# Optimization experiments

Measured on AMD Instinct MI355X. Metric: run time of the kernel, lower is better.

Reference implementation:

```python
import jax, jax.numpy as jnp
import numpy as np

INPUT, OUTPUT, HIDDEN, EMBED = 20000, 2048, 1024, 512
BATCH, NUM_GENES = 512, 20000

def _linear_init(key, fan_in, fan_out):
    kw, kb = jax.random.split(key)
    bound = 1.0 / np.sqrt(fan_in)
    W = jax.random.uniform(kw, (fan_out, fan_in), minval=-bound, maxval=bound, dtype=jnp.float32)
    b = jax.random.uniform(kb, (fan_out,), minval=-bound, maxval=bound, dtype=jnp.float32)
    return W, b

def setup_inputs() -> dict:
    key = jax.random.key(0)
    kx, ke, k1, k2, k3 = jax.random.split(key, 5)
    x = jax.random.normal(kx, (BATCH, INPUT), dtype=jnp.float32)
    embedding_x = jax.random.normal(ke, (NUM_GENES, EMBED), dtype=jnp.float32)
    W_ge, b_ge = _linear_init(k1, INPUT, HIDDEN)   # gene_expander Linear
    W_em, b_em = _linear_init(k2, EMBED, HIDDEN)   # embed_mlp Linear
    W_c, b_c = _linear_init(k3, 2 * HIDDEN, OUTPUT)  # combiner Linear
    return {"x": x, "embedding_x": embedding_x, "W_ge": W_ge, "b_ge": b_ge,
            "W_em": W_em, "b_em": b_em, "W_c": W_c, "b_c": b_c}

def reference(x, embedding_x, W_ge, b_ge, W_em, b_em, W_c, b_c):
    lrelu = lambda v: jax.nn.leaky_relu(v, negative_slope=0.01)
    # gene_expander: [B, input] -> [B, hidden]
    x_expanded = lrelu(x @ W_ge.T + b_ge)
    # embed_mlp (dropout = identity at eval): [G, embed] -> [G, hidden]
    gene_embeddings = lrelu(embedding_x @ W_em.T + b_em)
    # softmax over features, then batched GEMM replaces the per-sample loop
    num_genes = min(x.shape[1], gene_embeddings.shape[0])
    weights = jax.nn.softmax(x, axis=1)
    weighted_embeddings = weights[:, :num_genes] @ gene_embeddings[:num_genes]  # [B, hidden]
    combined = jnp.concatenate([x_expanded, weighted_embeddings], axis=1)  # [B, 2*hidden]
    return lrelu(combined @ W_c.T + b_c)  # [B, output]
```

## Files before the change

### kernel.cpp

```cpp
#include <hip/hip_runtime.h>
#include <hip/hip_bf16.h>
#include <stdint.h>

#define BATCH  512
#define INPUT  20000
#define KPAD   20032
#define NPADE  20224
#define HIDDEN 1024
#define EMBED  512
#define NOUT   2048

typedef __attribute__((ext_vector_type(8))) __bf16 bf16x8;
typedef __attribute__((ext_vector_type(8))) unsigned short u16x8;
typedef __attribute__((ext_vector_type(4))) unsigned short u16x4;
typedef __attribute__((ext_vector_type(4))) float f32x4;

static __device__ __forceinline__ unsigned short f2bf(float f) {
  uint32_t u = __builtin_bit_cast(uint32_t, f);
  u += 0x7fffu + ((u >> 16) & 1u);
  return (unsigned short)(u >> 16);
}

static __device__ __forceinline__ void g2l16(const unsigned short* g, unsigned short* l) {
  __builtin_amdgcn_global_load_lds(
      (const __attribute__((address_space(1))) void*)g,
      (__attribute__((address_space(3))) void*)l, 16, 0, 0);
}

#define MFMA(a, b, c) __builtin_amdgcn_mfma_f32_16x16x32_bf16((a), (b), (c), 0, 0, 0)

template<int EPI>
__global__ __launch_bounds__(512, 2) void gemm8r(
    const unsigned short* __restrict__ A0p, const unsigned short* __restrict__ B0p,
    const unsigned short* __restrict__ A1p, const unsigned short* __restrict__ B1p,
    int lda, int ldb,
    const float* __restrict__ bias,
    void* __restrict__ Cp, int ldc,
    int Nv, int Nw, int K, int kChunk)
{
  __shared__ __align__(16) unsigned short As[2][2][128 * 64];
  __shared__ __align__(16) unsigned short Bs[2][2][128 * 64];
  unsigned short* AsW = &As[0][0][0];
  unsigned short* BsW = &Bs[0][0][0];

  const int zall  = blockIdx.z;
  const int which = (EPI == 1) ? (zall >> 4) : 0;
  const int z     = (EPI == 1) ? (zall & 15) : 0;
  const unsigned short* Ap = which ? A1p : A0p;
  const unsigned short* Bp = which ? B1p : B0p;

  const int m0 = blockIdx.y * 256, n0 = blockIdx.x * 256;
  const int k0   = z * kChunk;
  const int kend = min(K, k0 + kChunk);
  const int nt   = (kend - k0) >> 6;

  const int tid = threadIdx.x;
  const int l = tid & 63, w = tid >> 6;
  const int srow = tid >> 3;
  const int sc8  = tid & 7;
  const unsigned short* agl = Ap + (size_t)(m0 + srow) * lda + k0 + sc8 * 8;
  const unsigned short* bgl = Bp + (size_t)(n0 + srow) * ldb + k0 + sc8 * 8;
  const int swc = ((sc8 ^ (srow & 7)) << 3);

  const int wr = w >> 2, wc = w & 3;
  const int lr = l & 15, lk = (l >> 4) * 8;
  const int xorv = (lr & 7) * 8;
  const int c0 = lk ^ xorv;
  const int c1 = (32 + lk) ^ xorv;

  auto ldsA = [&](int buf, int r) -> unsigned short* {
    return AsW + (buf * 2 + (r >> 7)) * 8192 + (r & 127) * 64 + swc;
  };
  auto ldsB = [&](int buf, int r) -> unsigned short* {
    return BsW + (buf * 2 + (r >> 7)) * 8192 + (r & 127) * 64 + swc;
  };
  auto rdA = [&](int buf, int mi, int ks) -> bf16x8 {
    return *reinterpret_cast<const bf16x8*>(
        AsW + (buf * 2 + wr) * 8192 + (mi * 16 + lr) * 64 + (ks ? c1 : c0));
  };
  auto rdB = [&](int buf, int ni, int ks) -> bf16x8 {
    return *reinterpret_cast<const bf16x8*>(
        BsW + (buf * 2 + (wc >> 1)) * 8192 + ((wc & 1) * 64 + ni * 16 + lr) * 64 + (ks ? c1 : c0));
  };

  f32x4 acc[8][4] = {};

  u16x8 ra0, ra1, ra2, ra3, rb0, rb1, rb2, rb3;

#define LOADT(dk)                                                            \
  do {                                                                       \
    ra0 = *reinterpret_cast<const u16x8*>(agl + (size_t)0   * lda + (dk));   \
    ra1 = *reinterpret_cast<const u16x8*>(agl + (size_t)64  * lda + (dk));   \
    ra2 = *reinterpret_cast<const u16x8*>(agl + (size_t)128 * lda + (dk));   \
    ra3 = *reinterpret_cast<const u16x8*>(agl + (size_t)192 * lda + (dk));   \
    rb0 = *reinterpret_cast<const u16x8*>(bgl + (size_t)0   * ldb + (dk));   \
    rb1 = *reinterpret_cast<const u16x8*>(bgl + (size_t)64  * ldb + (dk));   \
    rb2 = *reinterpret_cast<const u16x8*>(bgl + (size_t)128 * ldb + (dk));   \
    rb3 = *reinterpret_cast<const u16x8*>(bgl + (size_t)192 * ldb + (dk));   \
  } while (0)

#define WRITET(buf)                                                          \
  do {                                                                       \
    *reinterpret_cast<u16x8*>(ldsA(buf, srow))       = ra0;                  \
    *reinterpret_cast<u16x8*>(ldsA(buf, srow + 64))  = ra1;                  \
    *reinterpret_cast<u16x8*>(ldsA(buf, srow + 128)) = ra2;                  \
    *reinterpret_cast<u16x8*>(ldsA(buf, srow + 192)) = ra3;                  \
    *reinterpret_cast<u16x8*>(ldsB(buf, srow))       = rb0;                  \
    *reinterpret_cast<u16x8*>(ldsB(buf, srow + 64))  = rb1;                  \
    *reinterpret_cast<u16x8*>(ldsB(buf, srow + 128)) = rb2;                  \
    *reinterpret_cast<u16x8*>(ldsB(buf, srow + 192)) = rb3;                  \
  } while (0)

  LOADT(0);
  WRITET(0);
  __syncthreads();

  for (int t = 0; t < nt; ++t) {
    const int buf = t & 1, nb = buf ^ 1;
    if (t + 1 < nt) LOADT((t + 1) << 6);
    __builtin_amdgcn_sched_barrier(0);

    bf16x8 a[8][2], b[4][2];
#pragma unroll
    for (int mi = 0; mi < 8; ++mi) { a[mi][0] = rdA(buf, mi, 0); a[mi][1] = rdA(buf, mi, 1); }
#pragma unroll
    for (int ni = 0; ni < 4; ++ni) { b[ni][0] = rdB(buf, ni, 0); b[ni][1] = rdB(buf, ni, 1); }
#pragma unroll
    for (int mi = 0; mi < 8; ++mi)
#pragma unroll
      for (int ni = 0; ni < 4; ++ni) {
        acc[mi][ni] = MFMA(a[mi][0], b[ni][0], acc[mi][ni]);
        acc[mi][ni] = MFMA(a[mi][1], b[ni][1], acc[mi][ni]);
      }

    if (t + 1 < nt) WRITET(nb);
    __syncthreads();
  }
#undef LOADT
#undef WRITET

  const int rb_ = (l >> 4) * 4;
#pragma unroll
  for (int mi = 0; mi < 8; ++mi)
#pragma unroll
    for (int ni = 0; ni < 4; ++ni)
#pragma unroll
      for (int j = 0; j < 4; ++j) {
        int m = m0 + wr * 128 + mi * 16 + rb_ + j;
        int n = n0 + wc * 64 + ni * 16 + lr;
        float v = acc[mi][ni][j];
        if (EPI == 0) {
          if (n < Nw) {
            float t2 = v + bias[m];
            t2 = t2 > 0.f ? t2 : 0.01f * t2;
            reinterpret_cast<unsigned short*>(Cp)[(size_t)m * ldc + n] =
                (n < Nv) ? f2bf(t2) : (unsigned short)0;
          }
        } else {
          reinterpret_cast<float*>(Cp)[(size_t)z * (BATCH * NOUT) + (size_t)m * ldc +
                                       which * 1024 + n] = v;
        }
      }
}

template<int EPI>
__global__ __launch_bounds__(256) void gemm97(
    const unsigned short* __restrict__ A, const unsigned short* __restrict__ B,
    int lda, int ldb,
    const float* __restrict__ bias,
    void* __restrict__ Cp, int ldc, int pstride,
    int M, int N, int Nw, int K, int kChunk)
{
  __shared__ __align__(16) unsigned short As[128 * 64];
  __shared__ __align__(16) unsigned short Bs[128 * 64];

  const int z = blockIdx.z;
  const int m0 = blockIdx.y * 128, n0 = blockIdx.x * 128;
  const int k0   = z * kChunk;
  const int kend = min(K, k0 + kChunk);
  const int tid = threadIdx.x;
  const int l = tid & 63, w = tid >> 6;

  const int srow = w * 32 + (l >> 3);
  const int scol = (l & 7) * 8;
  const unsigned short* ag = A + (size_t)(m0 + srow) * lda + scol;
  const unsigned short* bg = B + (size_t)(n0 + srow) * ldb + scol;

  const int wm = (w >> 1) * 64, wn = (w & 1) * 64;
  const int lr = l & 15, lk = (l >> 4) * 8;

  f32x4 acc[4][4] = {};

  for (int kb = k0; kb < kend; kb += 64) {
#pragma unroll
    for (int j = 0; j < 4; ++j)
      g2l16(ag + (size_t)j * 8 * lda + kb, As + (w * 32 + j * 8) * 64);
#pragma unroll
    for (int j = 0; j < 4; ++j)
      g2l16(bg + (size_t)j * 8 * ldb + kb, Bs + (w * 32 + j * 8) * 64);
    __syncthreads();
#pragma unroll
    for (int ks = 0; ks < 2; ++ks) {
      bf16x8 a[4], b[4];
#pragma unroll
      for (int i = 0; i < 4; ++i)
        a[i] = *reinterpret_cast<const bf16x8*>(&As[(wm + i * 16 + lr) * 64 + ks * 32 + lk]);
#pragma unroll
      for (int i = 0; i < 4; ++i)
        b[i] = *reinterpret_cast<const bf16x8*>(&Bs[(wn + i * 16 + lr) * 64 + ks * 32 + lk]);
#pragma unroll
      for (int mi = 0; mi < 4; ++mi)
#pragma unroll
        for (int ni = 0; ni < 4; ++ni)
          acc[mi][ni] = MFMA(a[mi], b[ni], acc[mi][ni]);
    }
    __syncthreads();
  }

  const int rb = (l >> 4) * 4;
#pragma unroll
  for (int mi = 0; mi < 4; ++mi) {
#pragma unroll
    for (int ni = 0; ni < 4; ++ni) {
#pragma unroll
      for (int j = 0; j < 4; ++j) {
        int m = m0 + wm + mi * 16 + rb + j;
        int n = n0 + wn + ni * 16 + lr;
        float v = acc[mi][ni][j];
        if (EPI == 0) {
          if (n < Nw) {
            float t = v + bias[m];
            t = t > 0.f ? t : 0.01f * t;
            reinterpret_cast<unsigned short*>(Cp)[(size_t)m * ldc + n] =
                (n < N) ? f2bf(t) : (unsigned short)0;
          }
        } else {
          reinterpret_cast<float*>(Cp)[(size_t)z * pstride + (size_t)m * ldc + n] = v;
        }
      }
    }
  }
}

__global__ __launch_bounds__(256) void convert_kernel(
    const float* __restrict__ src, unsigned short* __restrict__ dst,
    int rows, int cols, int rowsPad, int colsPad)
{
  const int cpc = colsPad >> 3;
  const int nchunks = rowsPad * cpc;
  for (int idx = blockIdx.x * 256 + threadIdx.x; idx < nchunks; idx += gridDim.x * 256) {
    int row = idx / cpc;
    int c0  = (idx - row * cpc) << 3;
    u16x8 v = {};
    if (row < rows && c0 < cols) {
      const float* p = src + (size_t)row * cols + c0;
      f32x4 f0 = *reinterpret_cast<const f32x4*>(p);
      f32x4 f1 = *reinterpret_cast<const f32x4*>(p + 4);
      v[0] = f2bf(f0[0]); v[1] = f2bf(f0[1]); v[2] = f2bf(f0[2]); v[3] = f2bf(f0[3]);
      v[4] = f2bf(f1[0]); v[5] = f2bf(f1[1]); v[6] = f2bf(f1[2]); v[7] = f2bf(f1[3]);
    }
    *reinterpret_cast<u16x8*>(dst + (size_t)row * colsPad + c0) = v;
  }
}

__global__ __launch_bounds__(256) void prep_x_kernel(
    const float* __restrict__ x,
    unsigned short* __restrict__ xb,
    unsigned short* __restrict__ wb)
{
  const int r = blockIdx.x;
  const int t = threadIdx.x;
  const float* xr = x + (size_t)r * INPUT;

  float m = -3.4e38f, s = 0.f;
  for (int c = t; c < INPUT / 4; c += 256) {
    float4 v = reinterpret_cast<const float4*>(xr)[c];
    float cm = fmaxf(fmaxf(v.x, v.y), fmaxf(v.z, v.w));
    if (cm > m) { s *= __expf(m - cm); m = cm; }
    s += __expf(v.x - m) + __expf(v.y - m) + __expf(v.z - m) + __expf(v.w - m);
  }
#pragma unroll
  for (int off = 32; off > 0; off >>= 1) {
    float om = __shfl_xor(m, off);
    float os = __shfl_xor(s, off);
    float nm = fmaxf(m, om);
    s = s * __expf(m - nm) + os * __expf(om - nm);
    m = nm;
  }
  __shared__ float sm[4], ss[4];
  if ((t & 63) == 0) { sm[t >> 6] = m; ss[t >> 6] = s; }
  __syncthreads();
  float M4 = fmaxf(fmaxf(sm[0], sm[1]), fmaxf(sm[2], sm[3]));
  float S4 = ss[0] * __expf(sm[0] - M4) + ss[1] * __expf(sm[1] - M4)
           + ss[2] * __expf(sm[2] - M4) + ss[3] * __expf(sm[3] - M4);
  float inv = 1.f / S4;

  unsigned short* xbr = xb + (size_t)r * KPAD;
  unsigned short* wbr = wb + (size_t)r * KPAD;
  for (int c = t; c < KPAD / 4; c += 256) {
    u16x4 xo = {}, wo = {};
    if (c < INPUT / 4) {
      float4 v = reinterpret_cast<const float4*>(xr)[c];
      xo[0] = f2bf(v.x); xo[1] = f2bf(v.y); xo[2] = f2bf(v.z); xo[3] = f2bf(v.w);
      wo[0] = f2bf(__expf(v.x - M4) * inv);
      wo[1] = f2bf(__expf(v.y - M4) * inv);
      wo[2] = f2bf(__expf(v.z - M4) * inv);
      wo[3] = f2bf(__expf(v.w - M4) * inv);
    }
    reinterpret_cast<u16x4*>(xbr)[c] = xo;
    reinterpret_cast<u16x4*>(wbr)[c] = wo;
  }
}

template<int S, int MODE>
__global__ __launch_bounds__(256) void reduce_kernel(
    const float* __restrict__ P, const float* __restrict__ bias, void* __restrict__ outp)
{
  size_t base = ((size_t)blockIdx.x * 256 + threadIdx.x) * 4;
  f32x4 s = {};
#pragma unroll
  for (int zz = 0; zz < S; ++zz)
    s += *reinterpret_cast<const f32x4*>(P + (size_t)zz * BATCH * NOUT + base);
  int n = (int)(base & (NOUT - 1));
  if (MODE == 0) {
    u16x4 o;
    if (n < 1024) {
#pragma unroll
      for (int j = 0; j < 4; ++j) {
        float v = s[j] + bias[n + j];
        v = v > 0.f ? v : 0.01f * v;
        o[j] = f2bf(v);
      }
    } else {
#pragma unroll
      for (int j = 0; j < 4; ++j) o[j] = f2bf(s[j]);
    }
    *reinterpret_cast<u16x4*>(reinterpret_cast<unsigned short*>(outp) + base) = o;
  } else {
    f32x4 o;
#pragma unroll
    for (int j = 0; j < 4; ++j) {
      float v = s[j] + bias[n + j];
      o[j] = v > 0.f ? v : 0.01f * v;
    }
    *reinterpret_cast<f32x4*>(reinterpret_cast<float*>(outp) + base) = o;
  }
}

extern "C" void kernel_launch(void* const* d_in, const int* in_sizes, int n_in,
                              void* d_out, int out_size, void* d_ws, size_t ws_size,
                              hipStream_t stream)
{
  const float* x    = (const float*)d_in[0];
  const float* emb  = (const float*)d_in[1];
  const float* W_ge = (const float*)d_in[2];
  const float* b_ge = (const float*)d_in[3];
  const float* W_em = (const float*)d_in[4];
  const float* b_em = (const float*)d_in[5];
  const float* W_c  = (const float*)d_in[6];
  const float* b_c  = (const float*)d_in[7];
  float* out = (float*)d_out;

  char* ws = (char*)d_ws;
  unsigned short* xb   = (unsigned short*)(ws);
  unsigned short* wb   = (unsigned short*)(ws + 20512768);
  unsigned short* Wgeb = (unsigned short*)(ws + 41025536);
  unsigned short* Et   = (unsigned short*)(ws + 82051072);
  unsigned short* Wcb  = (unsigned short*)(ws + 123076608);
  unsigned short* comb = (unsigned short*)(ws + 131465216);
  float*          P    = (float*)(ws + 133562368);
  unsigned short* embb = (unsigned short*)(ws + 133562368);
  unsigned short* Wemb = (unsigned short*)(ws + 133562368 + 20709376);

  convert_kernel<<<1024, 256, 0, stream>>>(emb,  embb, INPUT, EMBED, NPADE, EMBED);
  convert_kernel<<<256,  256, 0, stream>>>(W_em, Wemb, HIDDEN, EMBED, HIDDEN, EMBED);
  convert_kernel<<<1024, 256, 0, stream>>>(W_ge, Wgeb, HIDDEN, INPUT, HIDDEN, KPAD);
  convert_kernel<<<512,  256, 0, stream>>>(W_c,  Wcb,  NOUT, NOUT, NOUT, NOUT);

  prep_x_kernel<<<BATCH, 256, 0, stream>>>(x, xb, wb);

  gemm8r<0><<<dim3(79, 4, 1), 512, 0, stream>>>(
      Wemb, embb, nullptr, nullptr, EMBED, EMBED, b_em,
      Et, KPAD, INPUT, KPAD, EMBED, EMBED);

  gemm8r<1><<<dim3(4, 2, 32), 512, 0, stream>>>(
      xb, Wgeb, wb, Et, KPAD, KPAD, nullptr,
      P, NOUT, 0, 0, KPAD, 1280);

  reduce_kernel<16, 0><<<(BATCH * NOUT / 4) / 256, 256, 0, stream>>>(P, b_ge, comb);

  gemm97<1><<<dim3(16, 4, 4), 256, 0, stream>>>(
      comb, Wcb, NOUT, NOUT, nullptr,
      P, NOUT, BATCH * NOUT, BATCH, NOUT, NOUT, NOUT, 512);

  reduce_kernel<4, 1><<<(BATCH * NOUT / 4) / 256, 256, 0, stream>>>(P, b_c, out);
}
```

Before: 241.7 us.

## Template GEMM on BK, remap blocks per XCD, and double-buffer register prefetch

Replaces the fixed 256x256x64 GEMM kernel with a template over K-tile depth and occupancy. It uses a 1D grid whose block index is remapped so tiles that share operands land on the same XCD. The main loop is unrolled by two with two register staging sets, so the global loads for tile t+2 are issued while tile t computes, and MFMA sections are wrapped in s_setprio. The embedding GEMM now uses BK=32 with 4 waves per SIMD. This adds register pressure and more complex code, and the XCD remap assumes round-robin dispatch of blocks across the 8 XCDs.

```diff
diff --git a/kernel.cpp b/kernel.cpp
--- a/kernel.cpp
+++ b/kernel.cpp
@@ -29,8 +29,8 @@
 
 #define MFMA(a, b, c) __builtin_amdgcn_mfma_f32_16x16x32_bf16((a), (b), (c), 0, 0, 0)
 
-template<int EPI>
-__global__ __launch_bounds__(512, 2) void gemm8r(
+template<int EPI, int BK, int MW>
+__global__ __launch_bounds__(512, MW) void gemmT(
     const unsigned short* __restrict__ A0p, const unsigned short* __restrict__ B0p,
     const unsigned short* __restrict__ A1p, const unsigned short* __restrict__ B1p,
     int lda, int ldb,
@@ -38,106 +38,118 @@
     void* __restrict__ Cp, int ldc,
     int Nv, int Nw, int K, int kChunk)
 {
-  __shared__ __align__(16) unsigned short As[2][2][128 * 64];
-  __shared__ __align__(16) unsigned short Bs[2][2][128 * 64];
-  unsigned short* AsW = &As[0][0][0];
-  unsigned short* BsW = &Bs[0][0][0];
-
-  const int zall  = blockIdx.z;
-  const int which = (EPI == 1) ? (zall >> 4) : 0;
-  const int z     = (EPI == 1) ? (zall & 15) : 0;
+  constexpr int CPR = BK / 8;
+  constexpr int RPP = 512 / CPR;
+  constexpr int NP  = 256 / RPP;
+  constexpr int KS  = BK / 32;
+  constexpr int XM  = CPR - 1;
+
+  __shared__ __align__(16) unsigned short AsW[2 * 256 * BK];
+  __shared__ __align__(16) unsigned short BsW[2 * 256 * BK];
+
+  const int b = blockIdx.x;
+  const int xcd = b & 7, rank = b >> 3;
+  int m0, n0, z = 0, which = 0;
+  if (EPI == 1) {
+    int g  = xcd + 8 * (rank >> 3);
+    int mm = rank & 7;
+    which = g >> 4; z = g & 15;
+    n0 = (mm >> 1) * 256; m0 = (mm & 1) * 256;
+  } else {
+    int x  = xcd + 8 * (rank >> 2);
+    int mm = rank & 3;
+    int nx = (Nw + 255) >> 8;
+    if (x >= nx) return;
+    n0 = x * 256; m0 = mm * 256;
+  }
   const unsigned short* Ap = which ? A1p : A0p;
   const unsigned short* Bp = which ? B1p : B0p;
 
-  const int m0 = blockIdx.y * 256, n0 = blockIdx.x * 256;
   const int k0   = z * kChunk;
   const int kend = min(K, k0 + kChunk);
-  const int nt   = (kend - k0) >> 6;
+  const int nt   = (kend - k0) / BK;
 
   const int tid = threadIdx.x;
   const int l = tid & 63, w = tid >> 6;
-  const int srow = tid >> 3;
-  const int sc8  = tid & 7;
+  const int srow = tid / CPR;
+  const int sc8  = tid % CPR;
   const unsigned short* agl = Ap + (size_t)(m0 + srow) * lda + k0 + sc8 * 8;
   const unsigned short* bgl = Bp + (size_t)(n0 + srow) * ldb + k0 + sc8 * 8;
-  const int swc = ((sc8 ^ (srow & 7)) << 3);
+  const int swc = ((sc8 ^ (srow & XM)) << 3);
 
   const int wr = w >> 2, wc = w & 3;
-  const int lr = l & 15, lk = (l >> 4) * 8;
-  const int xorv = (lr & 7) * 8;
-  const int c0 = lk ^ xorv;
-  const int c1 = (32 + lk) ^ xorv;
-
-  auto ldsA = [&](int buf, int r) -> unsigned short* {
-    return AsW + (buf * 2 + (r >> 7)) * 8192 + (r & 127) * 64 + swc;
-  };
-  auto ldsB = [&](int buf, int r) -> unsigned short* {
-    return BsW + (buf * 2 + (r >> 7)) * 8192 + (r & 127) * 64 + swc;
-  };
-  auto rdA = [&](int buf, int mi, int ks) -> bf16x8 {
-    return *reinterpret_cast<const bf16x8*>(
-        AsW + (buf * 2 + wr) * 8192 + (mi * 16 + lr) * 64 + (ks ? c1 : c0));
-  };
-  auto rdB = [&](int buf, int ni, int ks) -> bf16x8 {
-    return *reinterpret_cast<const bf16x8*>(
-        BsW + (buf * 2 + (wc >> 1)) * 8192 + ((wc & 1) * 64 + ni * 16 + lr) * 64 + (ks ? c1 : c0));
-  };
+  const int lr = l & 15, lkc = l >> 4;
 
   f32x4 acc[8][4] = {};
-
-  u16x8 ra0, ra1, ra2, ra3, rb0, rb1, rb2, rb3;
-
-#define LOADT(dk)                                                            \
-  do {                                                                       \
-    ra0 = *reinterpret_cast<const u16x8*>(agl + (size_t)0   * lda + (dk));   \
-    ra1 = *reinterpret_cast<const u16x8*>(agl + (size_t)64  * lda + (dk));   \
-    ra2 = *reinterpret_cast<const u16x8*>(agl + (size_t)128 * lda + (dk));   \
-    ra3 = *reinterpret_cast<const u16x8*>(agl + (size_t)192 * lda + (dk));   \
-    rb0 = *reinterpret_cast<const u16x8*>(bgl + (size_t)0   * ldb + (dk));   \
-    rb1 = *reinterpret_cast<const u16x8*>(bgl + (size_t)64  * ldb + (dk));   \
-    rb2 = *reinterpret_cast<const u16x8*>(bgl + (size_t)128 * ldb + (dk));   \
-    rb3 = *reinterpret_cast<const u16x8*>(bgl + (size_t)192 * ldb + (dk));   \
+  u16x8 rA[2][NP], rB[2][NP];
+
+#define LOADS(S, dk)                                                           \
+  do {                                                                         \
+    _Pragma("unroll")                                                          \
+    for (int p = 0; p < NP; ++p) {                                             \
+      rA[S][p] = *reinterpret_cast<const u16x8*>(agl + (size_t)(p * RPP) * lda + (dk)); \
+      rB[S][p] = *reinterpret_cast<const u16x8*>(bgl + (size_t)(p * RPP) * ldb + (dk)); \
+    }                                                                          \
   } while (0)
 
-#define WRITET(buf)                                                          \
-  do {                                                                       \
-    *reinterpret_cast<u16x8*>(ldsA(buf, srow))       = ra0;                  \
-    *reinterpret_cast<u16x8*>(ldsA(buf, srow + 64))  = ra1;                  \
-    *reinterpret_cast<u16x8*>(ldsA(buf, srow + 128)) = ra2;                  \
-    *reinterpret_cast<u16x8*>(ldsA(buf, srow + 192)) = ra3;                  \
-    *reinterpret_cast<u16x8*>(ldsB(buf, srow))       = rb0;                  \
-    *reinterpret_cast<u16x8*>(ldsB(buf, srow + 64))  = rb1;                  \
-    *reinterpret_cast<u16x8*>(ldsB(buf, srow + 128)) = rb2;                  \
-    *reinterpret_cast<u16x8*>(ldsB(buf, srow + 192)) = rb3;                  \
+#define WRITES(S, BUF)                                                         \
+  do {                                                                         \
+    _Pragma("unroll")                                                          \
+    for (int p = 0; p < NP; ++p) {                                             \
+      *reinterpret_cast<u16x8*>(AsW + (BUF) * (256 * BK) + (srow + p * RPP) * BK + swc) = rA[S][p]; \
+      *reinterpret_cast<u16x8*>(BsW + (BUF) * (256 * BK) + (srow + p * RPP) * BK + swc) = rB[S][p]; \
+    }                                                                          \
   } while (0)
 
-  LOADT(0);
-  WRITET(0);
+#define COMPUTE(BUF)                                                           \
+  do {                                                                         \
+    _Pragma("unroll")                                                          \
+    for (int ks = 0; ks < KS; ++ks) {                                          \
+      bf16x8 af[8], bg_[4];                                                    \
+      _Pragma("unroll")                                                        \
+      for (int mi = 0; mi < 8; ++mi) {                                         \
+        int ck = (ks * 4 + lkc) ^ (lr & XM);                                   \
+        af[mi] = *reinterpret_cast<const bf16x8*>(                             \
+            AsW + (BUF) * (256 * BK) + (wr * 128 + mi * 16 + lr) * BK + ck * 8); \
+      }                                                                        \
+      _Pragma("unroll")                                                        \
+      for (int ni = 0; ni < 4; ++ni) {                                         \
+        int ck = (ks * 4 + lkc) ^ (lr & XM);                                   \
+        bg_[ni] = *reinterpret_cast<const bf16x8*>(                            \
+            BsW + (BUF) * (256 * BK) + (wc * 64 + ni * 16 + lr) * BK + ck * 8); \
+      }                                                                        \
+      __builtin_amdgcn_s_setprio(1);                                           \
+      _Pragma("unroll")                                                        \
+      for (int mi = 0; mi < 8; ++mi)                                           \
+        _Pragma("unroll")                                                      \
+        for (int ni = 0; ni < 4; ++ni)                                         \
+          acc[mi][ni] = MFMA(af[mi], bg_[ni], acc[mi][ni]);                    \
+      __builtin_amdgcn_s_setprio(0);                                           \
+    }                                                                          \
+  } while (0)
+
+  LOADS(0, 0);
+  WRITES(0, 0);
+  if (nt > 1) LOADS(1, BK);
   __syncthreads();
 
-  for (int t = 0; t < nt; ++t) {
-    const int buf = t & 1, nb = buf ^ 1;
-    if (t + 1 < nt) LOADT((t + 1) << 6);
+  for (int t = 0; t < nt; t += 2) {
+    if (t + 2 < nt) LOADS(0, (t + 2) * BK);
     __builtin_amdgcn_sched_barrier(0);
-
-    bf16x8 a[8][2], b[4][2];
-#pragma unroll
-    for (int mi = 0; mi < 8; ++mi) { a[mi][0] = rdA(buf, mi, 0); a[mi][1] = rdA(buf, mi, 1); }
-#pragma unroll
-    for (int ni = 0; ni < 4; ++ni) { b[ni][0] = rdB(buf, ni, 0); b[ni][1] = rdB(buf, ni, 1); }
-#pragma unroll
-    for (int mi = 0; mi < 8; ++mi)
-#pragma unroll
-      for (int ni = 0; ni < 4; ++ni) {
-        acc[mi][ni] = MFMA(a[mi][0], b[ni][0], acc[mi][ni]);
-        acc[mi][ni] = MFMA(a[mi][1], b[ni][1], acc[mi][ni]);
-      }
-
-    if (t + 1 < nt) WRITET(nb);
+    COMPUTE(0);
+    if (t + 1 < nt) WRITES(1, 1);
     __syncthreads();
-  }
-#undef LOADT
-#undef WRITET
+    if (t + 1 < nt) {
+      if (t + 3 < nt) LOADS(1, (t + 3) * BK);
+      __builtin_amdgcn_sched_barrier(0);
+      COMPUTE(1);
+      if (t + 2 < nt) WRITES(0, 0);
+      __syncthreads();
+    }
+  }
+#undef LOADS
+#undef WRITES
+#undef COMPUTE
 
   const int rb_ = (l >> 4) * 4;
 #pragma unroll
@@ -201,18 +213,18 @@
     __syncthreads();
 #pragma unroll
     for (int ks = 0; ks < 2; ++ks) {
-      bf16x8 a[4], b[4];
+      bf16x8 a[4], b2[4];
 #pragma unroll
       for (int i = 0; i < 4; ++i)
         a[i] = *reinterpret_cast<const bf16x8*>(&As[(wm + i * 16 + lr) * 64 + ks * 32 + lk]);
 #pragma unroll
       for (int i = 0; i < 4; ++i)
-        b[i] = *reinterpret_cast<const bf16x8*>(&Bs[(wn + i * 16 + lr) * 64 + ks * 32 + lk]);
+        b2[i] = *reinterpret_cast<const bf16x8*>(&Bs[(wn + i * 16 + lr) * 64 + ks * 32 + lk]);
 #pragma unroll
       for (int mi = 0; mi < 4; ++mi)
 #pragma unroll
         for (int ni = 0; ni < 4; ++ni)
-          acc[mi][ni] = MFMA(a[mi], b[ni], acc[mi][ni]);
+          acc[mi][ni] = MFMA(a[mi], b2[ni], acc[mi][ni]);
     }
     __syncthreads();
   }
@@ -379,11 +391,11 @@
 
   prep_x_kernel<<<BATCH, 256, 0, stream>>>(x, xb, wb);
 
-  gemm8r<0><<<dim3(79, 4, 1), 512, 0, stream>>>(
+  gemmT<0, 32, 4><<<320, 512, 0, stream>>>(
       Wemb, embb, nullptr, nullptr, EMBED, EMBED, b_em,
       Et, KPAD, INPUT, KPAD, EMBED, EMBED);
 
-  gemm8r<1><<<dim3(4, 2, 32), 512, 0, stream>>>(
+  gemmT<1, 64, 2><<<256, 512, 0, stream>>>(
       xb, Wgeb, wb, Et, KPAD, KPAD, nullptr,
       P, NOUT, 0, 0, KPAD, 1280);
 
```

Result: slower. 589.4 us (+143.9%).

## Replace 256x256 GEMM tile with 128x256 K32 tile and XCD-aware block mapping

Applied to the files above, without the earlier changes.

The main GEMM kernel moves from 512 threads and 256x256 tiles with K=64 steps to 256 threads and 128x256 tiles with K=32 steps, which cuts LDS use and is meant to allow more resident blocks. Block indices are linearized and remapped so neighbouring tiles land on the same XCD, aiming at better L2 reuse. MFMA issue is bracketed with s_setprio. The cost is twice as many K iterations and barriers, plus less operand reuse per block.

```diff
diff --git a/kernel.cpp b/kernel.cpp
--- a/kernel.cpp
+++ b/kernel.cpp
@@ -30,7 +30,7 @@
 #define MFMA(a, b, c) __builtin_amdgcn_mfma_f32_16x16x32_bf16((a), (b), (c), 0, 0, 0)
 
 template<int EPI>
-__global__ __launch_bounds__(512, 2) void gemm8r(
+__global__ __launch_bounds__(256, 2) void gemmQ(
     const unsigned short* __restrict__ A0p, const unsigned short* __restrict__ B0p,
     const unsigned short* __restrict__ A1p, const unsigned short* __restrict__ B1p,
     int lda, int ldb,
@@ -38,77 +38,64 @@
     void* __restrict__ Cp, int ldc,
     int Nv, int Nw, int K, int kChunk)
 {
-  __shared__ __align__(16) unsigned short As[2][2][128 * 64];
-  __shared__ __align__(16) unsigned short Bs[2][2][128 * 64];
-  unsigned short* AsW = &As[0][0][0];
-  unsigned short* BsW = &Bs[0][0][0];
-
-  const int zall  = blockIdx.z;
-  const int which = (EPI == 1) ? (zall >> 4) : 0;
-  const int z     = (EPI == 1) ? (zall & 15) : 0;
+  __shared__ __align__(16) unsigned short AsW[2 * 128 * 32];
+  __shared__ __align__(16) unsigned short BsW[2 * 256 * 32];
+
+  const int b = blockIdx.x;
+  int m0, n0, z = 0, which = 0;
+  if (EPI == 1) {
+    int g = ((b >> 7) << 3) | (b & 7);
+    int j = (b >> 3) & 15;
+    which = g >> 4; z = g & 15;
+    m0 = (j & 3) * 128;
+    n0 = (j >> 2) * 256;
+  } else {
+    int xcd = b & 7, r = b >> 3;
+    int m = r / 10, q = r - m * 10;
+    int nidx = xcd + 8 * q;
+    if (nidx >= 79) return;
+    m0 = m * 128;
+    n0 = nidx * 256;
+  }
   const unsigned short* Ap = which ? A1p : A0p;
   const unsigned short* Bp = which ? B1p : B0p;
 
-  const int m0 = blockIdx.y * 256, n0 = blockIdx.x * 256;
   const int k0   = z * kChunk;
   const int kend = min(K, k0 + kChunk);
-  const int nt   = (kend - k0) >> 6;
+  const int nt   = (kend - k0) >> 5;
 
   const int tid = threadIdx.x;
   const int l = tid & 63, w = tid >> 6;
-  const int srow = tid >> 3;
-  const int sc8  = tid & 7;
+  const int srow = tid >> 2;
+  const int sc8  = tid & 3;
   const unsigned short* agl = Ap + (size_t)(m0 + srow) * lda + k0 + sc8 * 8;
   const unsigned short* bgl = Bp + (size_t)(n0 + srow) * ldb + k0 + sc8 * 8;
-  const int swc = ((sc8 ^ (srow & 7)) << 3);
-
-  const int wr = w >> 2, wc = w & 3;
-  const int lr = l & 15, lk = (l >> 4) * 8;
-  const int xorv = (lr & 7) * 8;
-  const int c0 = lk ^ xorv;
-  const int c1 = (32 + lk) ^ xorv;
-
-  auto ldsA = [&](int buf, int r) -> unsigned short* {
-    return AsW + (buf * 2 + (r >> 7)) * 8192 + (r & 127) * 64 + swc;
-  };
-  auto ldsB = [&](int buf, int r) -> unsigned short* {
-    return BsW + (buf * 2 + (r >> 7)) * 8192 + (r & 127) * 64 + swc;
-  };
-  auto rdA = [&](int buf, int mi, int ks) -> bf16x8 {
-    return *reinterpret_cast<const bf16x8*>(
-        AsW + (buf * 2 + wr) * 8192 + (mi * 16 + lr) * 64 + (ks ? c1 : c0));
-  };
-  auto rdB = [&](int buf, int ni, int ks) -> bf16x8 {
-    return *reinterpret_cast<const bf16x8*>(
-        BsW + (buf * 2 + (wc >> 1)) * 8192 + ((wc & 1) * 64 + ni * 16 + lr) * 64 + (ks ? c1 : c0));
-  };
+  const int swc = ((sc8 ^ ((srow >> 1) & 3)) << 3);
+
+  const int lr = l & 15, lkc = l >> 4;
+  const int ck = ((lkc ^ ((lr >> 1) & 3)) << 3);
 
   f32x4 acc[8][4] = {};
-
-  u16x8 ra0, ra1, ra2, ra3, rb0, rb1, rb2, rb3;
-
-#define LOADT(dk)                                                            \
-  do {                                                                       \
-    ra0 = *reinterpret_cast<const u16x8*>(agl + (size_t)0   * lda + (dk));   \
-    ra1 = *reinterpret_cast<const u16x8*>(agl + (size_t)64  * lda + (dk));   \
-    ra2 = *reinterpret_cast<const u16x8*>(agl + (size_t)128 * lda + (dk));   \
-    ra3 = *reinterpret_cast<const u16x8*>(agl + (size_t)192 * lda + (dk));   \
-    rb0 = *reinterpret_cast<const u16x8*>(bgl + (size_t)0   * ldb + (dk));   \
-    rb1 = *reinterpret_cast<const u16x8*>(bgl + (size_t)64  * ldb + (dk));   \
-    rb2 = *reinterpret_cast<const u16x8*>(bgl + (size_t)128 * ldb + (dk));   \
-    rb3 = *reinterpret_cast<const u16x8*>(bgl + (size_t)192 * ldb + (dk));   \
+  u16x8 ra0, ra1, rb0, rb1, rb2, rb3;
+
+#define LOADT(dk)                                                           \
+  do {                                                                      \
+    ra0 = *reinterpret_cast<const u16x8*>(agl + (size_t)0   * lda + (dk)); \
+    ra1 = *reinterpret_cast<const u16x8*>(agl + (size_t)64  * lda + (dk)); \
+    rb0 = *reinterpret_cast<const u16x8*>(bgl + (size_t)0   * ldb + (dk)); \
+    rb1 = *reinterpret_cast<const u16x8*>(bgl + (size_t)64  * ldb + (dk)); \
+    rb2 = *reinterpret_cast<const u16x8*>(bgl + (size_t)128 * ldb + (dk)); \
+    rb3 = *reinterpret_cast<const u16x8*>(bgl + (size_t)192 * ldb + (dk)); \
   } while (0)
 
-#define WRITET(buf)                                                          \
-  do {                                                                       \
-    *reinterpret_cast<u16x8*>(ldsA(buf, srow))       = ra0;                  \
-    *reinterpret_cast<u16x8*>(ldsA(buf, srow + 64))  = ra1;                  \
-    *reinterpret_cast<u16x8*>(ldsA(buf, srow + 128)) = ra2;                  \
-    *reinterpret_cast<u16x8*>(ldsA(buf, srow + 192)) = ra3;                  \
-    *reinterpret_cast<u16x8*>(ldsB(buf, srow))       = rb0;                  \
-    *reinterpret_cast<u16x8*>(ldsB(buf, srow + 64))  = rb1;                  \
-    *reinterpret_cast<u16x8*>(ldsB(buf, srow + 128)) = rb2;                  \
-    *reinterpret_cast<u16x8*>(ldsB(buf, srow + 192)) = rb3;                  \
+#define WRITET(BUF)                                                         \
+  do {                                                                      \
+    *reinterpret_cast<u16x8*>(AsW + (BUF)*4096 + (srow      ) * 32 + swc) = ra0; \
+    *reinterpret_cast<u16x8*>(AsW + (BUF)*4096 + (srow +  64) * 32 + swc) = ra1; \
+    *reinterpret_cast<u16x8*>(BsW + (BUF)*8192 + (srow      ) * 32 + swc) = rb0; \
+    *reinterpret_cast<u16x8*>(BsW + (BUF)*8192 + (srow +  64) * 32 + swc) = rb1; \
+    *reinterpret_cast<u16x8*>(BsW + (BUF)*8192 + (srow + 128) * 32 + swc) = rb2; \
+    *reinterpret_cast<u16x8*>(BsW + (BUF)*8192 + (srow + 192) * 32 + swc) = rb3; \
   } while (0)
 
   LOADT(0);
@@ -117,21 +104,25 @@
 
   for (int t = 0; t < nt; ++t) {
     const int buf = t & 1, nb = buf ^ 1;
-    if (t + 1 < nt) LOADT((t + 1) << 6);
+    if (t + 1 < nt) LOADT((t + 1) << 5);
     __builtin_amdgcn_sched_barrier(0);
 
-    bf16x8 a[8][2], b[4][2];
-#pragma unroll
-    for (int mi = 0; mi < 8; ++mi) { a[mi][0] = rdA(buf, mi, 0); a[mi][1] = rdA(buf, mi, 1); }
-#pragma unroll
-    for (int ni = 0; ni < 4; ++ni) { b[ni][0] = rdB(buf, ni, 0); b[ni][1] = rdB(buf, ni, 1); }
+    bf16x8 a[8], bfr[4];
 #pragma unroll
     for (int mi = 0; mi < 8; ++mi)
-#pragma unroll
-      for (int ni = 0; ni < 4; ++ni) {
-        acc[mi][ni] = MFMA(a[mi][0], b[ni][0], acc[mi][ni]);
-        acc[mi][ni] = MFMA(a[mi][1], b[ni][1], acc[mi][ni]);
-      }
+      a[mi] = *reinterpret_cast<const bf16x8*>(AsW + buf * 4096 + (mi * 16 + lr) * 32 + ck);
+#pragma unroll
+    for (int ni = 0; ni < 4; ++ni)
+      bfr[ni] = *reinterpret_cast<const bf16x8*>(
+          BsW + buf * 8192 + (w * 64 + ni * 16 + lr) * 32 + ck);
+
+    __builtin_amdgcn_s_setprio(1);
+#pragma unroll
+    for (int mi = 0; mi < 8; ++mi)
+#pragma unroll
+      for (int ni = 0; ni < 4; ++ni)
+        acc[mi][ni] = MFMA(a[mi], bfr[ni], acc[mi][ni]);
+    __builtin_amdgcn_s_setprio(0);
 
     if (t + 1 < nt) WRITET(nb);
     __syncthreads();
@@ -146,8 +137,8 @@
     for (int ni = 0; ni < 4; ++ni)
 #pragma unroll
       for (int j = 0; j < 4; ++j) {
-        int m = m0 + wr * 128 + mi * 16 + rb_ + j;
-        int n = n0 + wc * 64 + ni * 16 + lr;
+        int m = m0 + mi * 16 + rb_ + j;
+        int n = n0 + w * 64 + ni * 16 + lr;
         float v = acc[mi][ni][j];
         if (EPI == 0) {
           if (n < Nw) {
@@ -201,18 +192,18 @@
     __syncthreads();
 #pragma unroll
     for (int ks = 0; ks < 2; ++ks) {
-      bf16x8 a[4], b[4];
+      bf16x8 a[4], b2[4];
 #pragma unroll
       for (int i = 0; i < 4; ++i)
         a[i] = *reinterpret_cast<const bf16x8*>(&As[(wm + i * 16 + lr) * 64 + ks * 32 + lk]);
 #pragma unroll
       for (int i = 0; i < 4; ++i)
-        b[i] = *reinterpret_cast<const bf16x8*>(&Bs[(wn + i * 16 + lr) * 64 + ks * 32 + lk]);
+        b2[i] = *reinterpret_cast<const bf16x8*>(&Bs[(wn + i * 16 + lr) * 64 + ks * 32 + lk]);
 #pragma unroll
       for (int mi = 0; mi < 4; ++mi)
 #pragma unroll
         for (int ni = 0; ni < 4; ++ni)
-          acc[mi][ni] = MFMA(a[mi], b[ni], acc[mi][ni]);
+          acc[mi][ni] = MFMA(a[mi], b2[ni], acc[mi][ni]);
     }
     __syncthreads();
   }
@@ -379,11 +370,11 @@
 
   prep_x_kernel<<<BATCH, 256, 0, stream>>>(x, xb, wb);
 
-  gemm8r<0><<<dim3(79, 4, 1), 512, 0, stream>>>(
+  gemmQ<0><<<640, 256, 0, stream>>>(
       Wemb, embb, nullptr, nullptr, EMBED, EMBED, b_em,
       Et, KPAD, INPUT, KPAD, EMBED, EMBED);
 
-  gemm8r<1><<<dim3(4, 2, 32), 512, 0, stream>>>(
+  gemmQ<1><<<512, 256, 0, stream>>>(
       xb, Wgeb, wb, Et, KPAD, KPAD, nullptr,
       P, NOUT, 0, 0, KPAD, 1280);
 
```

Result: faster. 229.7 us (-5.0%).
